# Performance work log

Hardware: AMD Instinct MI355X
Metric: run time of the kernel (lower is better)

Reference implementation:

```python
import jax, jax.numpy as jnp
import numpy as np

B, S, H = 2, 2048, 2560
NH, NKV, D = 8, 4, 256
SW = 1024
EPS = 1e-6
NEG = -1e9


def _rms(x, w=None, eps=EPS):
    y = x * jax.lax.rsqrt(jnp.mean(x * x, axis=-1, keepdims=True) + eps)
    return y * (1.0 + w) if w is not None else y


def _rope(x, cos, sin):
    # x: [B, h, S, D]; cos/sin: [1, 1, S, D] with duplicated half-frequencies
    half = x.shape[-1] // 2
    out = x * cos
    o1 = out[..., :half] - x[..., half:] * sin[..., :half]
    o2 = out[..., half:] + x[..., :half] * sin[..., half:]
    return jnp.concatenate([o1, o2], axis=-1)


def setup_inputs() -> dict:
    key = jax.random.key(0)
    ks = jax.random.split(key, 6)
    hidden_states = jax.random.normal(ks[0], (B, S, H), dtype=jnp.float32)
    Wq = jax.random.normal(ks[1], (NH * D, H), dtype=jnp.float32) * 0.02
    Wk = jax.random.normal(ks[2], (NKV * D, H), dtype=jnp.float32) * 0.02
    Wv = jax.random.normal(ks[3], (NKV * D, H), dtype=jnp.float32) * 0.02
    Wo = jax.random.normal(ks[4], (H, NH * D), dtype=jnp.float32) * 0.02
    q_norm_w = jnp.zeros((D,), dtype=jnp.float32)
    k_norm_w = jnp.zeros((D,), dtype=jnp.float32)
    # RoPE tables (standard theta=10000, duplicated halves as in torch ref)
    pos = jnp.arange(S, dtype=jnp.float32)
    inv = 1.0 / (10000.0 ** (jnp.arange(0, D, 2, dtype=jnp.float32) / D))
    freqs = pos[:, None] * inv[None, :]            # [S, D/2]
    emb = jnp.concatenate([freqs, freqs], axis=-1)  # [S, D]
    cos = jnp.cos(emb)[None, None]                 # [1,1,S,D]
    sin = jnp.sin(emb)[None, None]
    # causal + sliding-window additive mask (allowed: i-SW < j <= i)
    i = jnp.arange(S)[:, None]
    j = jnp.arange(S)[None, :]
    allowed = (j <= i) & (j > i - SW)
    attention_mask = jnp.where(allowed, 0.0, NEG).astype(jnp.float32)[None, None]
    return {"hidden_states": hidden_states, "attention_mask": attention_mask,
            "cos": cos, "sin": sin, "Wq": Wq, "Wk": Wk, "Wv": Wv, "Wo": Wo,
            "q_norm_w": q_norm_w, "k_norm_w": k_norm_w}


def reference(hidden_states, attention_mask, cos, sin, Wq, Wk, Wv, Wo, q_norm_w, k_norm_w):
    b, s, _ = hidden_states.shape
    xq = (hidden_states @ Wq.T).reshape(b, s, NH, D).transpose(0, 2, 1, 3)  # [B,NH,S,D]
    xq = _rms(xq, q_norm_w)
    xk = (hidden_states @ Wk.T).reshape(b, s, NKV, D)
    xv = (hidden_states @ Wv.T).reshape(b, s, NKV, D)
    xk = _rms(xk, k_norm_w)
    xv = _rms(xv)  # parameterless rms_norm on v
    xk = xk.transpose(0, 2, 1, 3)  # [B,NKV,S,D]
    xv = xv.transpose(0, 2, 1, 3)
    xq = _rope(xq, cos, sin)
    xk = _rope(xk, cos, sin)
    # expand_kv path: S >= sliding_window and NH != NKV -> repeat_interleave
    g = NH // NKV
    xk = jnp.repeat(xk, g, axis=1)
    xv = jnp.repeat(xv, g, axis=1)
    # scale=1.0 in original (no 1/sqrt(d))
    scores = jnp.einsum('bhqd,bhkd->bhqk', xq, xk) + attention_mask
    attn = jax.nn.softmax(scores, axis=-1)
    out = jnp.einsum('bhqk,bhkd->bhqd', attn, xv)
    out = out.transpose(0, 2, 1, 3).reshape(b, s, NH * D)
    return out @ Wo.T
```

## Files before the change

### kernel.cpp

```cpp
#include <hip/hip_runtime.h>

#define B_   2
#define S_   2048
#define H_   2560
#define NH_  8
#define NKV_ 4
#define D_   256
#define SW_  1024

#define QKV_LD 4096

typedef __attribute__((ext_vector_type(8))) short    short8;
typedef __attribute__((ext_vector_type(8))) _Float16 half8;
typedef __attribute__((ext_vector_type(4))) _Float16 half4;
typedef __attribute__((ext_vector_type(4))) float    floatx4;
typedef __attribute__((ext_vector_type(2))) float    floatx2;

typedef unsigned int __attribute__((address_space(1))) as1_uint;
typedef unsigned int __attribute__((address_space(3))) as3_uint;

static __device__ __forceinline__ void async16(const void* g, void* l) {
    __builtin_amdgcn_global_load_lds((const as1_uint*)g, (as3_uint*)l, 16, 0, 0);
}

__global__ __launch_bounds__(256) void conv_all(
    const float* __restrict__ s0, const float* __restrict__ s1,
    const float* __restrict__ s2, const float* __restrict__ s3,
    const float* __restrict__ s4,
    _Float16* __restrict__ d0, _Float16* __restrict__ d1,
    _Float16* __restrict__ d2, _Float16* __restrict__ d3,
    _Float16* __restrict__ d4)
{
    const float* src; _Float16* dst; int n4;
    switch (blockIdx.y) {
        case 0:  src = s0; dst = d0; n4 = 4096 * 2560 / 4; break;
        case 1:  src = s1; dst = d1; n4 = 2048 * 2560 / 4; break;
        case 2:  src = s2; dst = d2; n4 = 1024 * 2560 / 4; break;
        case 3:  src = s3; dst = d3; n4 = 1024 * 2560 / 4; break;
        default: src = s4; dst = d4; n4 = 2560 * 2048 / 4; break;
    }
    for (int i = blockIdx.x * 256 + threadIdx.x; i < n4; i += gridDim.x * 256) {
        floatx4 v = *(const floatx4*)(src + (size_t)i * 4);
        half4 h = { (_Float16)v.x, (_Float16)v.y, (_Float16)v.z, (_Float16)v.w };
        *(half4*)(dst + (size_t)i * 4) = h;
    }
}

template <int C_FP32>
__global__ __launch_bounds__(512, 2) void gemm256(
    const _Float16* __restrict__ A,
    const _Float16* __restrict__ Bm,
    void* __restrict__ Cv,
    int M, int N, int K, int NBX)
{
    (void)M;
    __shared__ __align__(16) _Float16 As[2][256 * 64];
    __shared__ __align__(16) _Float16 Bs[2][256 * 64];

    const int tid  = threadIdx.x;
    const int lane = tid & 63, w = tid >> 6;
    const int wr = w >> 2, wc = w & 3;
    const int quad = lane >> 4, l16 = lane & 15;

    const int nwg = gridDim.x, cpx = nwg >> 3;
    const int swz = (blockIdx.x & 7) * cpx + (blockIdx.x >> 3);
    const int mBase = (swz / NBX) * 256, nBase = (swz % NBX) * 256;

    const int NT = K >> 6;

    const int stRow = w * 8 + (lane >> 3);
    const int stCol = (((lane & 7) ^ (lane >> 3)) << 3);
    const int rdsw  = (l16 & 7) << 3;

    const _Float16* Ag = A  + (size_t)mBase * K;
    const _Float16* Bg = Bm + (size_t)nBase * K;

    floatx4 acc[8][4];
    const floatx4 fz = {0.f, 0.f, 0.f, 0.f};
#pragma unroll
    for (int i = 0; i < 8; ++i)
#pragma unroll
        for (int j = 0; j < 4; ++j) acc[i][j] = fz;

    auto stA = [&](int tt, int h, _Float16* dst) {
#pragma unroll
        for (int r = 0; r < 2; ++r) {
            const int rb = h * 128 + r * 64;
            async16(Ag + (size_t)(rb + stRow) * K + tt * 64 + stCol,
                    dst + (size_t)(rb + w * 8) * 64);
        }
    };
    auto stB = [&](int tt, int h, _Float16* dst) {
#pragma unroll
        for (int r = 0; r < 2; ++r) {
            const int rb = h * 128 + r * 64;
            async16(Bg + (size_t)(rb + stRow) * K + tt * 64 + stCol,
                    dst + (size_t)(rb + w * 8) * 64);
        }
    };

    stA(0, 0, &As[0][0]); stA(0, 1, &As[0][0]);
    stB(0, 0, &Bs[0][0]); stB(0, 1, &Bs[0][0]);
    if (NT > 1) { stB(1, 0, &Bs[1][0]); stB(1, 1, &Bs[1][0]); }
    asm volatile("s_waitcnt vmcnt(4)" ::: "memory");
    __builtin_amdgcn_s_barrier();

    auto tile = [&](int t, _Float16* Ab, _Float16* Bb, _Float16* Ao) {
        half8 bf[4][2], af[2][2];
#pragma unroll
        for (int c = 0; c < 4; ++c) {
            const int brow = wc * 64 + c * 16 + l16;
#pragma unroll
            for (int s = 0; s < 2; ++s)
                bf[c][s] = *(const half8*)&Bb[(size_t)brow * 64 + ((s * 32 + quad * 8) ^ rdsw)];
        }
#pragma unroll
        for (int r = 0; r < 2; ++r) {
            const int arow = wr * 128 + r * 16 + l16;
#pragma unroll
            for (int s = 0; s < 2; ++s)
                af[r][s] = *(const half8*)&Ab[(size_t)arow * 64 + ((s * 32 + quad * 8) ^ rdsw)];
        }
        if (t + 1 < NT) stA(t + 1, 0, Ao);
        asm volatile("s_waitcnt lgkmcnt(8)");
        __builtin_amdgcn_s_barrier();
        asm volatile("s_waitcnt lgkmcnt(0)");
        __builtin_amdgcn_s_setprio(1);
#pragma unroll
        for (int s = 0; s < 2; ++s)
#pragma unroll
            for (int c = 0; c < 4; ++c) {
                acc[0][c] = __builtin_amdgcn_mfma_f32_16x16x32_f16(af[0][s], bf[c][s], acc[0][c], 0, 0, 0);
                acc[1][c] = __builtin_amdgcn_mfma_f32_16x16x32_f16(af[1][s], bf[c][s], acc[1][c], 0, 0, 0);
            }
        __builtin_amdgcn_s_setprio(0);
        __builtin_amdgcn_s_barrier();
#pragma unroll
        for (int p = 1; p < 4; ++p) {
#pragma unroll
            for (int r = 0; r < 2; ++r) {
                const int arow = wr * 128 + (2 * p + r) * 16 + l16;
#pragma unroll
                for (int s = 0; s < 2; ++s)
                    af[r][s] = *(const half8*)&Ab[(size_t)arow * 64 + ((s * 32 + quad * 8) ^ rdsw)];
            }
            if (p == 1)      { if (t + 1 < NT) stA(t + 1, 1, Ao); }
            else if (p == 2) { if (t + 2 < NT) stB(t + 2, 0, Bb); }
            else             { if (t + 2 < NT) stB(t + 2, 1, Bb); }
            __builtin_amdgcn_s_barrier();
            asm volatile("s_waitcnt lgkmcnt(0)");
            __builtin_amdgcn_s_setprio(1);
#pragma unroll
            for (int s = 0; s < 2; ++s)
#pragma unroll
                for (int c = 0; c < 4; ++c) {
                    acc[2 * p][c]     = __builtin_amdgcn_mfma_f32_16x16x32_f16(af[0][s], bf[c][s], acc[2 * p][c], 0, 0, 0);
                    acc[2 * p + 1][c] = __builtin_amdgcn_mfma_f32_16x16x32_f16(af[1][s], bf[c][s], acc[2 * p + 1][c], 0, 0, 0);
                }
            __builtin_amdgcn_s_setprio(0);
            if (p == 3) {
                if (t < NT - 2) asm volatile("s_waitcnt vmcnt(4)" ::: "memory");
                else            asm volatile("s_waitcnt vmcnt(0)" ::: "memory");
            }
            __builtin_amdgcn_s_barrier();
        }
    };

    for (int t = 0; t < NT; t += 2) {
        tile(t,     &As[0][0], &Bs[0][0], &As[1][0]);
        tile(t + 1, &As[1][0], &Bs[1][0], &As[0][0]);
    }

#pragma unroll
    for (int fr = 0; fr < 8; ++fr) {
        const int row0 = mBase + wr * 128 + fr * 16 + quad * 4;
#pragma unroll
        for (int c = 0; c < 4; ++c) {
            const int col = nBase + wc * 64 + c * 16 + l16;
#pragma unroll
            for (int r = 0; r < 4; ++r) {
                const size_t idx = (size_t)(row0 + r) * N + col;
                if (C_FP32) ((float*)Cv)[idx] = acc[fr][c][r];
                else        ((_Float16*)Cv)[idx] = (_Float16)acc[fr][c][r];
            }
        }
    }
}

__global__ __launch_bounds__(256) void rmsrope_inplace(
    _Float16* __restrict__ qkv,
    const float* __restrict__ cosT,
    const float* __restrict__ sinT,
    const float* __restrict__ qw,
    const float* __restrict__ kw)
{
    const int t = blockIdx.x;
    const int s = t & (S_ - 1);
    const int tid = threadIdx.x, lane = tid & 63, w = tid >> 6;
    _Float16* row = qkv + (size_t)t * QKV_LD;
    const int d0 = lane * 2, d1 = 128 + lane * 2;

    floatx2 c0 = *(const floatx2*)(cosT + (size_t)s * D_ + d0);
    floatx2 c1 = *(const floatx2*)(cosT + (size_t)s * D_ + d1);
    floatx2 s0 = *(const floatx2*)(sinT + (size_t)s * D_ + d0);
    floatx2 s1 = *(const floatx2*)(sinT + (size_t)s * D_ + d1);
    floatx2 qw0 = *(const floatx2*)(qw + d0), qw1 = *(const floatx2*)(qw + d1);
    floatx2 kw0 = *(const floatx2*)(kw + d0), kw1 = *(const floatx2*)(kw + d1);

#pragma unroll
    for (int p = 0; p < 4; ++p) {
        const int v = w + p * 4;
        _Float16* x = row + v * D_;
        float x0a = (float)x[d0], x0b = (float)x[d0 + 1];
        float x1a = (float)x[d1], x1b = (float)x[d1 + 1];
        float ss = x0a * x0a + x0b * x0b + x1a * x1a + x1b * x1b;
#pragma unroll
        for (int off = 32; off > 0; off >>= 1) ss += __shfl_xor(ss, off, 64);
        const float rinv = rsqrtf(ss * (1.0f / 256.0f) + 1e-6f);
        if (v < 8) {
            const float y0a = x0a * rinv * (1.f + qw0.x), y0b = x0b * rinv * (1.f + qw0.y);
            const float y1a = x1a * rinv * (1.f + qw1.x), y1b = x1b * rinv * (1.f + qw1.y);
            x[d0] = (_Float16)(y0a * c0.x - y1a * s0.x);
            x[d0 + 1] = (_Float16)(y0b * c0.y - y1b * s0.y);
            x[d1] = (_Float16)(y1a * c1.x + y0a * s1.x);
            x[d1 + 1] = (_Float16)(y1b * c1.y + y0b * s1.y);
        } else if (v < 12) {
            const float y0a = x0a * rinv * (1.f + kw0.x), y0b = x0b * rinv * (1.f + kw0.y);
            const float y1a = x1a * rinv * (1.f + kw1.x), y1b = x1b * rinv * (1.f + kw1.y);
            x[d0] = (_Float16)(y0a * c0.x - y1a * s0.x);
            x[d0 + 1] = (_Float16)(y0b * c0.y - y1b * s0.y);
            x[d1] = (_Float16)(y1a * c1.x + y0a * s1.x);
            x[d1 + 1] = (_Float16)(y1b * c1.y + y0b * s1.y);
        } else {
            x[d0] = (_Float16)(x0a * rinv);
            x[d0 + 1] = (_Float16)(x0b * rinv);
            x[d1] = (_Float16)(x1a * rinv);
            x[d1 + 1] = (_Float16)(x1b * rinv);
        }
    }
}

__global__ __launch_bounds__(256) void transpose_v(
    const _Float16* __restrict__ qkv, _Float16* __restrict__ Vt)
{
    __shared__ _Float16 tile[64][66];
    const int s0 = blockIdx.x * 64;
    const int dd0 = blockIdx.y * 64;
    const int bk = blockIdx.z;
    const int b = bk >> 2, kvh = bk & 3;
    const _Float16* src = qkv + (size_t)(b * S_) * QKV_LD + 3072 + kvh * D_;
    _Float16* dst = Vt + (size_t)bk * D_ * S_;
    const int tx = threadIdx.x & 63, ty = threadIdx.x >> 6;
    for (int r = ty; r < 64; r += 4)
        tile[r][tx] = src[(size_t)(s0 + r) * QKV_LD + dd0 + tx];
    __syncthreads();
    for (int r = ty; r < 64; r += 4)
        dst[(size_t)(dd0 + r) * S_ + s0 + tx] = tile[tx][r];
}

#define PS_STRIDE 40

__global__ __launch_bounds__(256, 2) void attn_kernel(
    const _Float16* __restrict__ qkv,
    const _Float16* __restrict__ Vt,
    _Float16* __restrict__ Oa)
{
    __shared__ __align__(16) _Float16 Ks[2][32 * 256];
    __shared__ __align__(16) _Float16 Vs[2][256 * 32];
    __shared__ __align__(16) _Float16 Ps[4][16 * PS_STRIDE];

    const int qb = blockIdx.x * 64;
    const int h = blockIdx.y, b = blockIdx.z;
    const int kvh = h >> 1;
    const int tid = threadIdx.x, lane = tid & 63, w = tid >> 6;
    const int quad = lane >> 4, l16 = lane & 15;

    const _Float16* Qrow = qkv + ((size_t)(b * S_ + qb + w * 16 + l16)) * QKV_LD + h * D_;
    half8 qf[8];
#pragma unroll
    for (int kst = 0; kst < 8; ++kst)
        qf[kst] = *(const half8*)(Qrow + kst * 32 + quad * 8);

    floatx4 o[16];
    const floatx4 fzero = {0.f, 0.f, 0.f, 0.f};
#pragma unroll
    for (int dt = 0; dt < 16; ++dt) o[dt] = fzero;
    float mrow[4] = {-1e30f, -1e30f, -1e30f, -1e30f};
    float lrow[4] = {0.f, 0.f, 0.f, 0.f};

    const _Float16* Kbase  = qkv + (size_t)(b * S_) * QKV_LD + 2048 + kvh * D_;
    const _Float16* Vtbase = Vt + (size_t)(b * NKV_ + kvh) * D_ * S_;
    const int kb_start = (qb >= SW_) ? qb - SW_ : 0;
    const int kb_end = qb + 32;

    auto stage = [&](int kb, int bufi) {
#pragma unroll
        for (int p = 0; p < 4; ++p) {
            const int keyl = w * 8 + p * 2 + (lane >> 5);
            const int g = ((lane & 31) - keyl) & 31;
            async16(Kbase + (size_t)(kb + keyl) * QKV_LD + g * 8,
                    &Ks[bufi][(w * 8 + p * 2) * 256]);
        }
#pragma unroll
        for (int p = 0; p < 4; ++p) {
            const int drow = w * 64 + p * 16 + (lane >> 2);
            const int q = lane & 3;
            async16(Vtbase + (size_t)drow * S_ + kb + q * 8,
                    &Vs[bufi][(w * 64 + p * 16) * 32]);
        }
    };

    int buf = 0;
    stage(kb_start, 0);

    for (int kb = kb_start; kb <= kb_end; kb += 32) {
        __syncthreads();
        if (kb + 32 <= kb_end) stage(kb + 32, buf ^ 1);

        floatx4 sacc[2];
        sacc[0] = fzero; sacc[1] = fzero;
#pragma unroll
        for (int jt = 0; jt < 2; ++jt) {
            const int keyl = jt * 16 + l16;
#pragma unroll
            for (int kst = 0; kst < 8; ++kst) {
                const int crot = (kst * 4 + quad + keyl) & 31;
                half8 kf = *(const half8*)&Ks[buf][keyl * 256 + crot * 8];
                sacc[jt] = __builtin_amdgcn_mfma_f32_16x16x32_f16(qf[kst], kf, sacc[jt], 0, 0, 0);
            }
        }

        const int q0 = qb + w * 16 + quad * 4;
        float sval[2][4], tmax[4];
#pragma unroll
        for (int r = 0; r < 4; ++r) tmax[r] = -1e30f;
#pragma unroll
        for (int jt = 0; jt < 2; ++jt) {
            const int kg = kb + jt * 16 + l16;
#pragma unroll
            for (int r = 0; r < 4; ++r) {
                const int qg = q0 + r;
                const bool ok = (kg <= qg) && (kg + SW_ > qg);
                const float vv = ok ? sacc[jt][r] : -1e30f;
                sval[jt][r] = vv;
                tmax[r] = fmaxf(tmax[r], vv);
            }
        }
#pragma unroll
        for (int r = 0; r < 4; ++r) {
#pragma unroll
            for (int off = 1; off < 16; off <<= 1)
                tmax[r] = fmaxf(tmax[r], __shfl_xor(tmax[r], off, 64));
            const float mnew = fmaxf(mrow[r], tmax[r]);
            const float alpha = __expf(mrow[r] - mnew);
            mrow[r] = mnew;
            lrow[r] *= alpha;
            tmax[r] = alpha;
        }
        float rsum[4] = {0.f, 0.f, 0.f, 0.f};
#pragma unroll
        for (int jt = 0; jt < 2; ++jt)
#pragma unroll
            for (int r = 0; r < 4; ++r) {
                float pv = __expf(sval[jt][r] - mrow[r]);
                pv = (sval[jt][r] <= -1e29f) ? 0.0f : pv;
                rsum[r] += pv;
                Ps[w][(quad * 4 + r) * PS_STRIDE + jt * 16 + l16] = (_Float16)pv;
            }
#pragma unroll
        for (int r = 0; r < 4; ++r) {
#pragma unroll
            for (int off = 1; off < 16; off <<= 1)
                rsum[r] += __shfl_xor(rsum[r], off, 64);
            lrow[r] += rsum[r];
        }
#pragma unroll
        for (int dt = 0; dt < 16; ++dt)
#pragma unroll
            for (int r = 0; r < 4; ++r) o[dt][r] *= tmax[r];

        half8 pa = *(const half8*)&Ps[w][l16 * PS_STRIDE + quad * 8];
#pragma unroll
        for (int dt = 0; dt < 16; ++dt) {
            half8 vf = *(const half8*)&Vs[buf][(dt * 16 + l16) * 32 + quad * 8];
            o[dt] = __builtin_amdgcn_mfma_f32_16x16x32_f16(pa, vf, o[dt], 0, 0, 0);
        }
        buf ^= 1;
    }

    const int qrow = qb + w * 16 + quad * 4;
#pragma unroll
    for (int r = 0; r < 4; ++r) {
        const float inv = (lrow[r] > 0.f) ? (1.0f / lrow[r]) : 0.f;
        _Float16* orow = Oa + ((size_t)(b * S_ + qrow + r)) * (NH_ * D_) + h * D_;
#pragma unroll
        for (int dt = 0; dt < 16; ++dt)
            orow[dt * 16 + l16] = (_Float16)(o[dt][r] * inv);
    }
}

extern "C" void kernel_launch(void* const* d_in, const int* in_sizes, int n_in,
                              void* d_out, int out_size, void* d_ws, size_t ws_size,
                              hipStream_t stream)
{
    (void)in_sizes; (void)n_in; (void)out_size; (void)ws_size;
    const float* hid  = (const float*)d_in[0];
    const float* cosT = (const float*)d_in[2];
    const float* sinT = (const float*)d_in[3];
    const float* Wq   = (const float*)d_in[4];
    const float* Wk   = (const float*)d_in[5];
    const float* Wv   = (const float*)d_in[6];
    const float* Wo   = (const float*)d_in[7];
    const float* qw   = (const float*)d_in[8];
    const float* kw   = (const float*)d_in[9];
    float* out = (float*)d_out;

    char* ws = (char*)d_ws;
    _Float16* qkv  = (_Float16*)(ws);
    _Float16* attn = (_Float16*)(ws + 33554432ull);
    _Float16* hidH = (_Float16*)(ws + 50331648ull);
    _Float16* wQKV = (_Float16*)(ws + 71303168ull);
    _Float16* woH  = (_Float16*)(ws + 92274688ull);
    _Float16* Vt   = (_Float16*)(ws + 102760448ull);

    conv_all<<<dim3(512, 5), 256, 0, stream>>>(
        hid, Wq, Wk, Wv, Wo,
        hidH, wQKV, wQKV + (size_t)2048 * 2560, wQKV + (size_t)3072 * 2560, woH);

    gemm256<0><<<dim3(256), 512, 0, stream>>>(hidH, wQKV, qkv, 4096, 4096, 2560, 16);
    rmsrope_inplace<<<4096, 256, 0, stream>>>(qkv, cosT, sinT, qw, kw);
    transpose_v<<<dim3(32, 4, 8), 256, 0, stream>>>(qkv, Vt);
    attn_kernel<<<dim3(32, 8, 2), 256, 0, stream>>>(qkv, Vt, attn);
    gemm256<1><<<dim3(160), 512, 0, stream>>>(attn, woH, out, 4096, 2560, 2048, 10);
}
```

Baseline: 415.6 us.

## Enlarge attention tiles to 128 queries x 64 keys with lazy rescale and skipping

The attention kernel now gives each block 128 queries (32 per wave, two MFMA row tiles) and streams K/V in 64-key blocks, so every K/V fragment loaded from LDS feeds two MFMAs. It adds an XOR swizzle on the V tile, a block-index swizzle for scheduling, per-wave skipping of fully masked key blocks, s_setprio around the MFMA sections, and a lazy online-softmax rescale that updates the max only when it grows by more than 8. The aim is to cut LDS traffic and softmax overhead per FLOP. In exchange, register and LDS use rise to one block per CU with only 256 blocks, so occupancy and load balance drop, and the lazy max threshold slightly changes numerical behaviour.

```diff
diff --git a/kernel.cpp b/kernel.cpp
--- a/kernel.cpp
+++ b/kernel.cpp
@@ -258,145 +258,191 @@
         dst[(size_t)(dd0 + r) * S_ + s0 + tx] = tile[tx][r];
 }
 
-#define PS_STRIDE 40
-
-__global__ __launch_bounds__(256, 2) void attn_kernel(
+#define KVB_ 64
+#define PS_STRIDE 72
+
+__global__ __launch_bounds__(256, 1) void attn_kernel(
     const _Float16* __restrict__ qkv,
     const _Float16* __restrict__ Vt,
     _Float16* __restrict__ Oa)
 {
-    __shared__ __align__(16) _Float16 Ks[2][32 * 256];
-    __shared__ __align__(16) _Float16 Vs[2][256 * 32];
-    __shared__ __align__(16) _Float16 Ps[4][16 * PS_STRIDE];
-
-    const int qb = blockIdx.x * 64;
-    const int h = blockIdx.y, b = blockIdx.z;
+    __shared__ __align__(16) _Float16 Ks[2][KVB_ * 256];
+    __shared__ __align__(16) _Float16 Vs[2][256 * KVB_];
+    __shared__ __align__(16) _Float16 Ps[4][32 * PS_STRIDE];
+
+    const int idx = blockIdx.x;
+    const int swz = (idx & 7) * 32 + (idx >> 3);
+    const int qt = swz & 15, h = (swz >> 4) & 7, b = swz >> 7;
+    const int qb = qt * 128;
     const int kvh = h >> 1;
+
     const int tid = threadIdx.x, lane = tid & 63, w = tid >> 6;
     const int quad = lane >> 4, l16 = lane & 15;
-
-    const _Float16* Qrow = qkv + ((size_t)(b * S_ + qb + w * 16 + l16)) * QKV_LD + h * D_;
-    half8 qf[8];
-#pragma unroll
-    for (int kst = 0; kst < 8; ++kst)
-        qf[kst] = *(const half8*)(Qrow + kst * 32 + quad * 8);
-
-    floatx4 o[16];
+    const int q0 = qb + w * 32;
+
+    half8 qf[2][8];
+#pragma unroll
+    for (int mi = 0; mi < 2; ++mi) {
+        const _Float16* Qrow = qkv + ((size_t)(b * S_ + q0 + mi * 16 + l16)) * QKV_LD + h * D_;
+#pragma unroll
+        for (int kst = 0; kst < 8; ++kst)
+            qf[mi][kst] = *(const half8*)(Qrow + kst * 32 + quad * 8);
+    }
+
+    floatx4 o[2][16];
     const floatx4 fzero = {0.f, 0.f, 0.f, 0.f};
 #pragma unroll
-    for (int dt = 0; dt < 16; ++dt) o[dt] = fzero;
-    float mrow[4] = {-1e30f, -1e30f, -1e30f, -1e30f};
-    float lrow[4] = {0.f, 0.f, 0.f, 0.f};
+    for (int mi = 0; mi < 2; ++mi)
+#pragma unroll
+        for (int dt = 0; dt < 16; ++dt) o[mi][dt] = fzero;
+    float mrow[2][4], lrow[2][4];
+#pragma unroll
+    for (int mi = 0; mi < 2; ++mi)
+#pragma unroll
+        for (int r = 0; r < 4; ++r) { mrow[mi][r] = -50000.f; lrow[mi][r] = 0.f; }
 
     const _Float16* Kbase  = qkv + (size_t)(b * S_) * QKV_LD + 2048 + kvh * D_;
     const _Float16* Vtbase = Vt + (size_t)(b * NKV_ + kvh) * D_ * S_;
     const int kb_start = (qb >= SW_) ? qb - SW_ : 0;
-    const int kb_end = qb + 32;
+    const int kb_end = qb + 64;
 
     auto stage = [&](int kb, int bufi) {
 #pragma unroll
-        for (int p = 0; p < 4; ++p) {
-            const int keyl = w * 8 + p * 2 + (lane >> 5);
+        for (int p = 0; p < 8; ++p) {
+            const int keyl = w * 16 + p * 2 + (lane >> 5);
             const int g = ((lane & 31) - keyl) & 31;
             async16(Kbase + (size_t)(kb + keyl) * QKV_LD + g * 8,
-                    &Ks[bufi][(w * 8 + p * 2) * 256]);
-        }
-#pragma unroll
-        for (int p = 0; p < 4; ++p) {
-            const int drow = w * 64 + p * 16 + (lane >> 2);
-            const int q = lane & 3;
-            async16(Vtbase + (size_t)drow * S_ + kb + q * 8,
-                    &Vs[bufi][(w * 64 + p * 16) * 32]);
+                    &Ks[bufi][(w * 16 + p * 2) * 256]);
+        }
+#pragma unroll
+        for (int p = 0; p < 8; ++p) {
+            const int drow = w * 64 + p * 8 + (lane >> 3);
+            const int sc = (lane & 7) ^ ((lane >> 3) & 7);
+            async16(Vtbase + (size_t)drow * S_ + kb + sc * 8,
+                    &Vs[bufi][(w * 64 + p * 8) * KVB_]);
         }
     };
 
     int buf = 0;
     stage(kb_start, 0);
 
-    for (int kb = kb_start; kb <= kb_end; kb += 32) {
+    for (int kb = kb_start; kb <= kb_end; kb += KVB_) {
         __syncthreads();
-        if (kb + 32 <= kb_end) stage(kb + 32, buf ^ 1);
-
-        floatx4 sacc[2];
-        sacc[0] = fzero; sacc[1] = fzero;
-#pragma unroll
-        for (int jt = 0; jt < 2; ++jt) {
-            const int keyl = jt * 16 + l16;
-#pragma unroll
-            for (int kst = 0; kst < 8; ++kst) {
-                const int crot = (kst * 4 + quad + keyl) & 31;
-                half8 kf = *(const half8*)&Ks[buf][keyl * 256 + crot * 8];
-                sacc[jt] = __builtin_amdgcn_mfma_f32_16x16x32_f16(qf[kst], kf, sacc[jt], 0, 0, 0);
-            }
-        }
-
-        const int q0 = qb + w * 16 + quad * 4;
-        float sval[2][4], tmax[4];
-#pragma unroll
-        for (int r = 0; r < 4; ++r) tmax[r] = -1e30f;
-#pragma unroll
-        for (int jt = 0; jt < 2; ++jt) {
-            const int kg = kb + jt * 16 + l16;
-#pragma unroll
-            for (int r = 0; r < 4; ++r) {
-                const int qg = q0 + r;
-                const bool ok = (kg <= qg) && (kg + SW_ > qg);
-                const float vv = ok ? sacc[jt][r] : -1e30f;
-                sval[jt][r] = vv;
-                tmax[r] = fmaxf(tmax[r], vv);
-            }
-        }
+        if (kb + KVB_ <= kb_end) stage(kb + KVB_, buf ^ 1);
+
+        if ((kb <= q0 + 31) && (kb + KVB_ - 1 >= q0 - (SW_ - 1))) {
+            floatx4 sacc[4][2];
+#pragma unroll
+            for (int jt = 0; jt < 4; ++jt) { sacc[jt][0] = fzero; sacc[jt][1] = fzero; }
+            __builtin_amdgcn_s_setprio(1);
+#pragma unroll
+            for (int jt = 0; jt < 4; ++jt) {
+                const int keyl = jt * 16 + l16;
+#pragma unroll
+                for (int kst = 0; kst < 8; ++kst) {
+                    const int crot = (kst * 4 + quad + keyl) & 31;
+                    half8 kf = *(const half8*)&Ks[buf][keyl * 256 + crot * 8];
+                    sacc[jt][0] = __builtin_amdgcn_mfma_f32_16x16x32_f16(qf[0][kst], kf, sacc[jt][0], 0, 0, 0);
+                    sacc[jt][1] = __builtin_amdgcn_mfma_f32_16x16x32_f16(qf[1][kst], kf, sacc[jt][1], 0, 0, 0);
+                }
+            }
+            __builtin_amdgcn_s_setprio(0);
+
+            float sval[4][2][4], tmax[2][4];
+#pragma unroll
+            for (int mi = 0; mi < 2; ++mi)
+#pragma unroll
+                for (int r = 0; r < 4; ++r) tmax[mi][r] = -1e30f;
+#pragma unroll
+            for (int jt = 0; jt < 4; ++jt) {
+                const int kg = kb + jt * 16 + l16;
+#pragma unroll
+                for (int mi = 0; mi < 2; ++mi)
+#pragma unroll
+                    for (int r = 0; r < 4; ++r) {
+                        const int qg = q0 + mi * 16 + quad * 4 + r;
+                        const bool ok = (unsigned)(qg - kg) < (unsigned)SW_;
+                        const float vv = ok ? sacc[jt][mi][r] : -1e30f;
+                        sval[jt][mi][r] = vv;
+                        tmax[mi][r] = fmaxf(tmax[mi][r], vv);
+                    }
+            }
+            float alpha[2][4];
+            bool need = false;
+#pragma unroll
+            for (int mi = 0; mi < 2; ++mi)
+#pragma unroll
+                for (int r = 0; r < 4; ++r) {
+                    float t = tmax[mi][r];
+#pragma unroll
+                    for (int off = 1; off < 16; off <<= 1)
+                        t = fmaxf(t, __shfl_xor(t, off, 64));
+                    const float mold = mrow[mi][r];
+                    const float mnew = (t > mold + 8.f) ? t : mold;
+                    alpha[mi][r] = __expf(mold - mnew);
+                    need |= (mnew != mold);
+                    mrow[mi][r] = mnew;
+                    lrow[mi][r] *= alpha[mi][r];
+                }
+            if (__any(need)) {
+#pragma unroll
+                for (int mi = 0; mi < 2; ++mi)
+#pragma unroll
+                    for (int dt = 0; dt < 16; ++dt)
+#pragma unroll
+                        for (int r = 0; r < 4; ++r) o[mi][dt][r] *= alpha[mi][r];
+            }
+            float rsum[2][4] = {{0.f, 0.f, 0.f, 0.f}, {0.f, 0.f, 0.f, 0.f}};
+#pragma unroll
+            for (int jt = 0; jt < 4; ++jt)
+#pragma unroll
+                for (int mi = 0; mi < 2; ++mi)
+#pragma unroll
+                    for (int r = 0; r < 4; ++r) {
+                        const float pv = __expf(sval[jt][mi][r] - mrow[mi][r]);
+                        rsum[mi][r] += pv;
+                        Ps[w][(mi * 16 + quad * 4 + r) * PS_STRIDE + jt * 16 + l16] = (_Float16)pv;
+                    }
+#pragma unroll
+            for (int mi = 0; mi < 2; ++mi)
+#pragma unroll
+                for (int r = 0; r < 4; ++r) {
+                    float s = rsum[mi][r];
+#pragma unroll
+                    for (int off = 1; off < 16; off <<= 1)
+                        s += __shfl_xor(s, off, 64);
+                    lrow[mi][r] += s;
+                }
+
+            __builtin_amdgcn_s_setprio(1);
+#pragma unroll
+            for (int ks = 0; ks < 2; ++ks) {
+                half8 pa0 = *(const half8*)&Ps[w][(l16) * PS_STRIDE + ks * 32 + quad * 8];
+                half8 pa1 = *(const half8*)&Ps[w][(16 + l16) * PS_STRIDE + ks * 32 + quad * 8];
+#pragma unroll
+                for (int dt = 0; dt < 16; ++dt) {
+                    const int row = dt * 16 + l16;
+                    half8 vf = *(const half8*)&Vs[buf][row * KVB_ + (((ks * 4 + quad) ^ (l16 & 7)) * 8)];
+                    o[0][dt] = __builtin_amdgcn_mfma_f32_16x16x32_f16(pa0, vf, o[0][dt], 0, 0, 0);
+                    o[1][dt] = __builtin_amdgcn_mfma_f32_16x16x32_f16(pa1, vf, o[1][dt], 0, 0, 0);
+                }
+            }
+            __builtin_amdgcn_s_setprio(0);
+        }
+        buf ^= 1;
+    }
+
+#pragma unroll
+    for (int mi = 0; mi < 2; ++mi)
 #pragma unroll
         for (int r = 0; r < 4; ++r) {
-#pragma unroll
-            for (int off = 1; off < 16; off <<= 1)
-                tmax[r] = fmaxf(tmax[r], __shfl_xor(tmax[r], off, 64));
-            const float mnew = fmaxf(mrow[r], tmax[r]);
-            const float alpha = __expf(mrow[r] - mnew);
-            mrow[r] = mnew;
-            lrow[r] *= alpha;
-            tmax[r] = alpha;
-        }
-        float rsum[4] = {0.f, 0.f, 0.f, 0.f};
-#pragma unroll
-        for (int jt = 0; jt < 2; ++jt)
-#pragma unroll
-            for (int r = 0; r < 4; ++r) {
-                float pv = __expf(sval[jt][r] - mrow[r]);
-                pv = (sval[jt][r] <= -1e29f) ? 0.0f : pv;
-                rsum[r] += pv;
-                Ps[w][(quad * 4 + r) * PS_STRIDE + jt * 16 + l16] = (_Float16)pv;
-            }
-#pragma unroll
-        for (int r = 0; r < 4; ++r) {
-#pragma unroll
-            for (int off = 1; off < 16; off <<= 1)
-                rsum[r] += __shfl_xor(rsum[r], off, 64);
-            lrow[r] += rsum[r];
-        }
-#pragma unroll
-        for (int dt = 0; dt < 16; ++dt)
-#pragma unroll
-            for (int r = 0; r < 4; ++r) o[dt][r] *= tmax[r];
-
-        half8 pa = *(const half8*)&Ps[w][l16 * PS_STRIDE + quad * 8];
-#pragma unroll
-        for (int dt = 0; dt < 16; ++dt) {
-            half8 vf = *(const half8*)&Vs[buf][(dt * 16 + l16) * 32 + quad * 8];
-            o[dt] = __builtin_amdgcn_mfma_f32_16x16x32_f16(pa, vf, o[dt], 0, 0, 0);
-        }
-        buf ^= 1;
-    }
-
-    const int qrow = qb + w * 16 + quad * 4;
-#pragma unroll
-    for (int r = 0; r < 4; ++r) {
-        const float inv = (lrow[r] > 0.f) ? (1.0f / lrow[r]) : 0.f;
-        _Float16* orow = Oa + ((size_t)(b * S_ + qrow + r)) * (NH_ * D_) + h * D_;
-#pragma unroll
-        for (int dt = 0; dt < 16; ++dt)
-            orow[dt * 16 + l16] = (_Float16)(o[dt][r] * inv);
-    }
+            const int qrow = q0 + mi * 16 + quad * 4 + r;
+            const float inv = (lrow[mi][r] > 0.f) ? (1.0f / lrow[mi][r]) : 0.f;
+            _Float16* orow = Oa + ((size_t)(b * S_ + qrow)) * (NH_ * D_) + h * D_;
+#pragma unroll
+            for (int dt = 0; dt < 16; ++dt)
+                orow[dt * 16 + l16] = (_Float16)(o[mi][dt][r] * inv);
+        }
 }
 
 extern "C" void kernel_launch(void* const* d_in, const int* in_sizes, int n_in,
@@ -430,6 +476,6 @@
     gemm256<0><<<dim3(256), 512, 0, stream>>>(hidH, wQKV, qkv, 4096, 4096, 2560, 16);
     rmsrope_inplace<<<4096, 256, 0, stream>>>(qkv, cosT, sinT, qw, kw);
     transpose_v<<<dim3(32, 4, 8), 256, 0, stream>>>(qkv, Vt);
-    attn_kernel<<<dim3(32, 8, 2), 256, 0, stream>>>(qkv, Vt, attn);
+    attn_kernel<<<dim3(256), 256, 0, stream>>>(qkv, Vt, attn);
     gemm256<1><<<dim3(160), 512, 0, stream>>>(attn, woH, out, 4096, 2560, 2048, 10);
 }
```

Measured after the change: 422.8 us. No clear change (+1.7%).

## Skip fully masked key tiles per wave and use lazy softmax rescaling

Applied to the files above, without the earlier changes.

Each wave now skips the QK, softmax and PV work for key tiles that lie entirely outside its 16-row causal sliding window. It adds lazy max updates (only rescale when the new max exceeds the old by more than 8) with a wave-wide __any check to skip the output rescale loop. It also removes the masked-value zeroing branch by starting the running max at -50000, and raises wave priority around the MFMA loops with s_setprio. The lazy threshold lets exponentials exceed 1 by up to e^8 before rescaling, which puts more pressure on fp16 P values and fp32 accumulators.

```diff
diff --git a/kernel.cpp b/kernel.cpp
--- a/kernel.cpp
+++ b/kernel.cpp
@@ -274,8 +274,9 @@
     const int kvh = h >> 1;
     const int tid = threadIdx.x, lane = tid & 63, w = tid >> 6;
     const int quad = lane >> 4, l16 = lane & 15;
-
-    const _Float16* Qrow = qkv + ((size_t)(b * S_ + qb + w * 16 + l16)) * QKV_LD + h * D_;
+    const int q0 = qb + w * 16;
+
+    const _Float16* Qrow = qkv + ((size_t)(b * S_ + q0 + l16)) * QKV_LD + h * D_;
     half8 qf[8];
 #pragma unroll
     for (int kst = 0; kst < 8; ++kst)
@@ -285,7 +286,7 @@
     const floatx4 fzero = {0.f, 0.f, 0.f, 0.f};
 #pragma unroll
     for (int dt = 0; dt < 16; ++dt) o[dt] = fzero;
-    float mrow[4] = {-1e30f, -1e30f, -1e30f, -1e30f};
+    float mrow[4] = {-50000.f, -50000.f, -50000.f, -50000.f};
     float lrow[4] = {0.f, 0.f, 0.f, 0.f};
 
     const _Float16* Kbase  = qkv + (size_t)(b * S_) * QKV_LD + 2048 + kvh * D_;
@@ -317,78 +318,89 @@
         __syncthreads();
         if (kb + 32 <= kb_end) stage(kb + 32, buf ^ 1);
 
-        floatx4 sacc[2];
-        sacc[0] = fzero; sacc[1] = fzero;
-#pragma unroll
-        for (int jt = 0; jt < 2; ++jt) {
-            const int keyl = jt * 16 + l16;
-#pragma unroll
-            for (int kst = 0; kst < 8; ++kst) {
-                const int crot = (kst * 4 + quad + keyl) & 31;
-                half8 kf = *(const half8*)&Ks[buf][keyl * 256 + crot * 8];
-                sacc[jt] = __builtin_amdgcn_mfma_f32_16x16x32_f16(qf[kst], kf, sacc[jt], 0, 0, 0);
-            }
-        }
-
-        const int q0 = qb + w * 16 + quad * 4;
-        float sval[2][4], tmax[4];
-#pragma unroll
-        for (int r = 0; r < 4; ++r) tmax[r] = -1e30f;
-#pragma unroll
-        for (int jt = 0; jt < 2; ++jt) {
-            const int kg = kb + jt * 16 + l16;
+        if ((kb <= q0 + 15) && (kb + 31 >= q0 - (SW_ - 1))) {
+            floatx4 sacc[2];
+            sacc[0] = fzero; sacc[1] = fzero;
+            __builtin_amdgcn_s_setprio(1);
+#pragma unroll
+            for (int jt = 0; jt < 2; ++jt) {
+                const int keyl = jt * 16 + l16;
+#pragma unroll
+                for (int kst = 0; kst < 8; ++kst) {
+                    const int crot = (kst * 4 + quad + keyl) & 31;
+                    half8 kf = *(const half8*)&Ks[buf][keyl * 256 + crot * 8];
+                    sacc[jt] = __builtin_amdgcn_mfma_f32_16x16x32_f16(qf[kst], kf, sacc[jt], 0, 0, 0);
+                }
+            }
+            __builtin_amdgcn_s_setprio(0);
+
+            const int qq0 = q0 + quad * 4;
+            float sval[2][4], tmax[4];
+#pragma unroll
+            for (int r = 0; r < 4; ++r) tmax[r] = -1e30f;
+#pragma unroll
+            for (int jt = 0; jt < 2; ++jt) {
+                const int kg = kb + jt * 16 + l16;
+#pragma unroll
+                for (int r = 0; r < 4; ++r) {
+                    const int qg = qq0 + r;
+                    const bool ok = (unsigned)(qg - kg) < (unsigned)SW_;
+                    const float vv = ok ? sacc[jt][r] : -1e30f;
+                    sval[jt][r] = vv;
+                    tmax[r] = fmaxf(tmax[r], vv);
+                }
+            }
+            float alpha[4];
+            bool need = false;
 #pragma unroll
             for (int r = 0; r < 4; ++r) {
-                const int qg = q0 + r;
-                const bool ok = (kg <= qg) && (kg + SW_ > qg);
-                const float vv = ok ? sacc[jt][r] : -1e30f;
-                sval[jt][r] = vv;
-                tmax[r] = fmaxf(tmax[r], vv);
-            }
-        }
-#pragma unroll
-        for (int r = 0; r < 4; ++r) {
-#pragma unroll
-            for (int off = 1; off < 16; off <<= 1)
-                tmax[r] = fmaxf(tmax[r], __shfl_xor(tmax[r], off, 64));
-            const float mnew = fmaxf(mrow[r], tmax[r]);
-            const float alpha = __expf(mrow[r] - mnew);
-            mrow[r] = mnew;
-            lrow[r] *= alpha;
-            tmax[r] = alpha;
-        }
-        float rsum[4] = {0.f, 0.f, 0.f, 0.f};
-#pragma unroll
-        for (int jt = 0; jt < 2; ++jt)
+                float t = tmax[r];
+#pragma unroll
+                for (int off = 1; off < 16; off <<= 1)
+                    t = fmaxf(t, __shfl_xor(t, off, 64));
+                const float mold = mrow[r];
+                const float mnew = (t > mold + 8.f) ? t : mold;
+                alpha[r] = __expf(mold - mnew);
+                need |= (mnew != mold);
+                mrow[r] = mnew;
+                lrow[r] *= alpha[r];
+            }
+            if (__any(need)) {
+#pragma unroll
+                for (int dt = 0; dt < 16; ++dt)
+#pragma unroll
+                    for (int r = 0; r < 4; ++r) o[dt][r] *= alpha[r];
+            }
+            float rsum[4] = {0.f, 0.f, 0.f, 0.f};
+#pragma unroll
+            for (int jt = 0; jt < 2; ++jt)
+#pragma unroll
+                for (int r = 0; r < 4; ++r) {
+                    const float pv = __expf(sval[jt][r] - mrow[r]);
+                    rsum[r] += pv;
+                    Ps[w][(quad * 4 + r) * PS_STRIDE + jt * 16 + l16] = (_Float16)pv;
+                }
 #pragma unroll
             for (int r = 0; r < 4; ++r) {
-                float pv = __expf(sval[jt][r] - mrow[r]);
-                pv = (sval[jt][r] <= -1e29f) ? 0.0f : pv;
-                rsum[r] += pv;
-                Ps[w][(quad * 4 + r) * PS_STRIDE + jt * 16 + l16] = (_Float16)pv;
-            }
-#pragma unroll
-        for (int r = 0; r < 4; ++r) {
-#pragma unroll
-            for (int off = 1; off < 16; off <<= 1)
-                rsum[r] += __shfl_xor(rsum[r], off, 64);
-            lrow[r] += rsum[r];
-        }
-#pragma unroll
-        for (int dt = 0; dt < 16; ++dt)
-#pragma unroll
-            for (int r = 0; r < 4; ++r) o[dt][r] *= tmax[r];
-
-        half8 pa = *(const half8*)&Ps[w][l16 * PS_STRIDE + quad * 8];
-#pragma unroll
-        for (int dt = 0; dt < 16; ++dt) {
-            half8 vf = *(const half8*)&Vs[buf][(dt * 16 + l16) * 32 + quad * 8];
-            o[dt] = __builtin_amdgcn_mfma_f32_16x16x32_f16(pa, vf, o[dt], 0, 0, 0);
+#pragma unroll
+                for (int off = 1; off < 16; off <<= 1)
+                    rsum[r] += __shfl_xor(rsum[r], off, 64);
+                lrow[r] += rsum[r];
+            }
+
+            half8 pa = *(const half8*)&Ps[w][l16 * PS_STRIDE + quad * 8];
+            __builtin_amdgcn_s_setprio(1);
+#pragma unroll
+            for (int dt = 0; dt < 16; ++dt) {
+                half8 vf = *(const half8*)&Vs[buf][(dt * 16 + l16) * 32 + quad * 8];
+                o[dt] = __builtin_amdgcn_mfma_f32_16x16x32_f16(pa, vf, o[dt], 0, 0, 0);
+            }
+            __builtin_amdgcn_s_setprio(0);
         }
         buf ^= 1;
     }
 
-    const int qrow = qb + w * 16 + quad * 4;
+    const int qrow = q0 + quad * 4;
 #pragma unroll
     for (int r = 0; r < 4; ++r) {
         const float inv = (lrow[r] > 0.f) ? (1.0f / lrow[r]) : 0.f;
```

After: 414.1 us. About the same (-0.4%).
